# Performance work log

Hardware: AMD Instinct MI355X
Metric: run time of the kernel (lower is better)

The kernel has to match this reference:

```python
import jax, jax.numpy as jnp
import numpy as np
from jax import lax

GAMMA = 1.0  # init kwarg

def setup_inputs() -> dict:
    key = jax.random.key(0)
    k1, k2 = jax.random.split(key)
    B, L, D = 64, 256, 1024
    return {
        "student_tokens": jax.random.normal(k1, (B, L, D), jnp.float32),
        "teacher_tokens": jax.random.normal(k2, (B, L, D), jnp.float32),
    }

def _soft_dtw(dist, gamma):
    # dist: (B, LS, LT). Returns R[:, LS, LT] of the soft-DTW DP.
    B, LS, LT = dist.shape
    inf = jnp.array(jnp.inf, dist.dtype)

    def cell(r_left, inputs):
        d, r_diag, r_up = inputs  # each (B,)
        stacked = jnp.stack([r_diag, r_up, r_left], axis=-1)  # (B, 3)
        softmin = -gamma * jax.nn.logsumexp(-stacked / gamma, axis=-1)
        r = d + softmin
        return r, r

    def row_step(prev_row, dist_row):
        # prev_row: (B, LT+1) = R[i-1, :]; dist_row: (B, LT) = dist[:, i-1, :]
        xs = (dist_row.T, prev_row[:, :-1].T, prev_row[:, 1:].T)  # each (LT, B)
        r0 = jnp.full((B,), inf, dist.dtype)  # R[i, 0] = inf
        _, row = lax.scan(cell, r0, xs)  # (LT, B)
        new_row = jnp.concatenate([r0[:, None], row.T], axis=1)  # (B, LT+1)
        return new_row, None

    init_row = jnp.concatenate(
        [jnp.zeros((B, 1), dist.dtype), jnp.full((B, LT), inf, dist.dtype)], axis=1
    )  # R[0, :] = [0, inf, ..., inf]
    final_row, _ = lax.scan(row_step, init_row, jnp.swapaxes(dist, 0, 1))
    return final_row[:, -1]  # R[:, LS, LT]

def reference(student_tokens, teacher_tokens):
    # torch.cdist(p=2) via the expanded quadratic form (avoids (B,L,L,D) blowup)
    s2 = jnp.sum(student_tokens * student_tokens, axis=-1)  # (B, LS)
    t2 = jnp.sum(teacher_tokens * teacher_tokens, axis=-1)  # (B, LT)
    sq = (s2[:, :, None] + t2[:, None, :]
          - 2.0 * jnp.einsum('bld,bmd->blm', student_tokens, teacher_tokens))
    dist = jnp.sqrt(jnp.maximum(sq, 1e-12))  # (B, LS, LT)
    return _soft_dtw(dist, GAMMA).mean()
```

## Files before the change

### kernel.cpp

```cpp
#include <hip/hip_runtime.h>
#include <math.h>

#define BB 64
#define LL 256
#define DD 1024
#define NDPAD 512
#define BK 32
#define LOG2E 1.4426950408889634f
#define LN2   0.6931471805599453f

typedef __attribute__((ext_vector_type(8))) short short8v;
typedef __attribute__((ext_vector_type(4))) float float4v;

__device__ __forceinline__ unsigned short f2bf(float f) {
    unsigned u = __float_as_uint(f);
    unsigned r = (u + 0x7fffu + ((u >> 16) & 1u)) >> 16;
    return (unsigned short)r;
}
__device__ __forceinline__ float bf2f(unsigned short u) {
    return __uint_as_float(((unsigned)u) << 16);
}

__global__ __launch_bounds__(512) void fused_kernel(const float* __restrict__ S,
                                                    const float* __restrict__ T,
                                                    unsigned short* __restrict__ Dd) {
    __shared__ unsigned short lds[2][2][2][128 * BK];
    __shared__ float nrmP[2][2][128];

    const int b    = blockIdx.x;
    const int tile = blockIdx.y;
    const int i0 = (tile & 1) * 128;
    const int j0 = (tile >> 1) * 128;
    const int tid = threadIdx.x, w = tid >> 6, lane = tid & 63;
    const int p = w >> 2;
    const int q = w & 3;
    const int wr = q >> 1, wc = q & 1;
    const int kbase = p * 512;

    const float* Sg = S + ((size_t)b * LL + i0) * DD;
    const float* Tg = T + ((size_t)b * LL + j0) * DD;

    const int sr   = q * 16 + (lane >> 2);
    const int slot = lane & 3;
    const int kb   = slot ^ (sr & 3);

    float4v acc[4][4];
    const float4v fzero = {0.f, 0.f, 0.f, 0.f};
    #pragma unroll
    for (int mi = 0; mi < 4; ++mi)
        #pragma unroll
        for (int ni = 0; ni < 4; ++ni) acc[mi][ni] = fzero;

    struct Stg { float4 a[2][2]; float4 bb[2][2]; };
    Stg st0, st1;
    float ns[2][2] = {};

    auto issue = [&](Stg& s, int kt) {
        const float* pa = Sg + (size_t)sr * DD + kbase + kt * BK + kb * 8;
        const float* pb = Tg + (size_t)sr * DD + kbase + kt * BK + kb * 8;
        s.a[0][0]  = *(const float4*)(pa);
        s.a[0][1]  = *(const float4*)(pa + 4);
        s.a[1][0]  = *(const float4*)(pa + 64 * DD);
        s.a[1][1]  = *(const float4*)(pa + 64 * DD + 4);
        s.bb[0][0] = *(const float4*)(pb);
        s.bb[0][1] = *(const float4*)(pb + 4);
        s.bb[1][0] = *(const float4*)(pb + 64 * DD);
        s.bb[1][1] = *(const float4*)(pb + 64 * DD + 4);
    };

    auto cvtwrite = [&](const float4& v0, const float4& v1, unsigned short* dst, float& nacc) {
        nacc += v0.x * v0.x + v0.y * v0.y + v0.z * v0.z + v0.w * v0.w
              + v1.x * v1.x + v1.y * v1.y + v1.z * v1.z + v1.w * v1.w;
        uint4 o;
        o.x = ((unsigned)f2bf(v0.y) << 16) | f2bf(v0.x);
        o.y = ((unsigned)f2bf(v0.w) << 16) | f2bf(v0.z);
        o.z = ((unsigned)f2bf(v1.y) << 16) | f2bf(v1.x);
        o.w = ((unsigned)f2bf(v1.w) << 16) | f2bf(v1.z);
        *(uint4*)dst = o;
    };

    auto commit = [&](Stg& s, int buf) {
        #pragma unroll
        for (int n = 0; n < 2; ++n) {
            cvtwrite(s.a[n][0],  s.a[n][1],  &lds[p][buf][0][(n * 64 + sr) * BK + slot * 8], ns[0][n]);
            cvtwrite(s.bb[n][0], s.bb[n][1], &lds[p][buf][1][(n * 64 + sr) * BK + slot * 8], ns[1][n]);
        }
    };

    auto compute = [&](int buf) {
        const unsigned short* LA = &lds[p][buf][0][0];
        const unsigned short* LB = &lds[p][buf][1][0];
        short8v af[4], bf[4];
        #pragma unroll
        for (int mi = 0; mi < 4; ++mi) {
            int row = wr * 64 + mi * 16 + (lane & 15);
            int kbf = (lane >> 4) ^ (row & 3);
            af[mi] = *(const short8v*)(LA + row * BK + kbf * 8);
        }
        #pragma unroll
        for (int ni = 0; ni < 4; ++ni) {
            int row = wc * 64 + ni * 16 + (lane & 15);
            int kbf = (lane >> 4) ^ (row & 3);
            bf[ni] = *(const short8v*)(LB + row * BK + kbf * 8);
        }
        #pragma unroll
        for (int mi = 0; mi < 4; ++mi)
            #pragma unroll
            for (int ni = 0; ni < 4; ++ni)
                acc[mi][ni] = __builtin_amdgcn_mfma_f32_16x16x32_bf16(af[mi], bf[ni],
                                                                      acc[mi][ni], 0, 0, 0);
    };

    issue(st0, 0);
    for (int kt2 = 0; kt2 < 16; kt2 += 2) {
        issue(st1, kt2 + 1);
        commit(st0, 0);
        __syncthreads();
        compute(0);
        if (kt2 + 2 < 16) issue(st0, kt2 + 2);
        commit(st1, 1);
        __syncthreads();
        compute(1);
    }

    #pragma unroll
    for (int side = 0; side < 2; ++side)
        #pragma unroll
        for (int n = 0; n < 2; ++n) {
            float s = ns[side][n];
            s += __shfl_xor(s, 1, 64);
            s += __shfl_xor(s, 2, 64);
            if (slot == 0) nrmP[p][side][n * 64 + sr] = s;
        }
    __syncthreads();

    float* cb = (float*)&lds[0][0][0][0];
    if (p == 1) {
        #pragma unroll
        for (int mi = 0; mi < 4; ++mi)
            #pragma unroll
            for (int ni = 0; ni < 4; ++ni)
                *(float4v*)(cb + q * 4096 + (mi * 4 + ni) * 256 + lane * 4) = acc[mi][ni];
    }
    __syncthreads();

    if (p == 0) {
        #pragma unroll
        for (int mi = 0; mi < 4; ++mi)
            #pragma unroll
            for (int ni = 0; ni < 4; ++ni)
                acc[mi][ni] += *(const float4v*)(cb + q * 4096 + (mi * 4 + ni) * 256 + lane * 4);

        const int r0 = (lane >> 4) * 4;
        const int cf = lane & 15;
        unsigned short* Db = Dd + (size_t)b * NDPAD * 256;
        #pragma unroll
        for (int mi = 0; mi < 4; ++mi) {
            #pragma unroll
            for (int ni = 0; ni < 4; ++ni) {
                int lj = wc * 64 + ni * 16 + cf;
                float tj = nrmP[0][1][lj] + nrmP[1][1][lj];
                int j = j0 + lj;
                #pragma unroll
                for (int rg = 0; rg < 4; ++rg) {
                    int li = wr * 64 + mi * 16 + r0 + rg;
                    float sq = nrmP[0][0][li] + nrmP[1][0][li] + tj - 2.0f * acc[mi][ni][rg];
                    float dv = sqrtf(fmaxf(sq, 1e-12f));
                    int i = i0 + li;
                    Db[(size_t)(i + j) * 256 + j] = f2bf(dv * LOG2E);
                }
            }
        }
    }
}


__device__ __forceinline__ float wshr1(float src, float fill) {
    return __int_as_float(__builtin_amdgcn_update_dpp(
        __float_as_int(fill), __float_as_int(src), 0x138, 0xF, 0xF, false));
}

__global__ __launch_bounds__(256) void sdtw_kernel(const unsigned short* __restrict__ Dg,
                                                   float* __restrict__ res) {
    __shared__ unsigned short sd[8][16 * 256];
    __shared__ float bbuf[3][2][16];
    const int b = blockIdx.x;
    const int tid = threadIdx.x;
    const int w = tid >> 6;
    const int lane = tid & 63;
    const float INF = INFINITY;
    const unsigned short* Db = Dg + (size_t)b * NDPAD * 256;

    auto prefetch = [&](int c) {
        #pragma unroll
        for (int q = 0; q < 8; ++q) {
            __builtin_amdgcn_global_load_lds(
                (const __attribute__((address_space(1))) void*)(Db + (size_t)c * 4096 + q * 512 + lane * 8),
                (__attribute__((address_space(3))) void*)(&sd[c & 7][q * 512]),
                16, 0, 0);
        }
    };

    const int col0 = 64 * w + lane;
    float rm1 = INF, rm2 = INF;
    float p2carry = (tid == 0) ? 0.0f : INF;
    float bcarry = INF;

    if (w == 0) {
        prefetch(0);
        prefetch(1);
        asm volatile("s_waitcnt vmcnt(8)" ::: "memory");
    }
    asm volatile("s_waitcnt lgkmcnt(0)" ::: "memory");
    __builtin_amdgcn_s_barrier();

    for (int r = 0; r < 35; ++r) {
        if (w == 0 && r + 2 < 32) prefetch(r + 2);
        const int c = r - w;
        if (0 <= c && c < 32) {
            const unsigned short* Lp = &sd[c & 7][0];
            float dv[16];
            #pragma unroll
            for (int q = 0; q < 16; ++q)
                dv[q] = bf2f(Lp[q * 256 + col0]);

            float bv[16];
            if (w == 0) {
                #pragma unroll
                for (int q = 0; q < 16; ++q) bv[q] = INF;
            } else {
                const float4* bp4 = (const float4*)&bbuf[w - 1][c & 1][0];
                float4 b0 = bp4[0], b1 = bp4[1], b2 = bp4[2], b3 = bp4[3];
                bv[0] = bcarry;
                bv[1] = b0.x;  bv[2] = b0.y;  bv[3] = b0.z;  bv[4] = b0.w;
                bv[5] = b1.x;  bv[6] = b1.y;  bv[7] = b1.z;  bv[8] = b1.w;
                bv[9] = b2.x;  bv[10] = b2.y; bv[11] = b2.z; bv[12] = b2.w;
                bv[13] = b3.x; bv[14] = b3.y; bv[15] = b3.z;
                bcarry = b3.w;
            }
            asm volatile("s_waitcnt lgkmcnt(0)" ::: "memory");
            __builtin_amdgcn_sched_barrier(0);

            const int ibase = 16 * c - col0;
            float bb[16];
            #pragma unroll
            for (int q = 0; q < 16; ++q) {
                float p1 = wshr1(rm1, bv[q]);
                float p2 = p2carry;
                p2carry = p1;
                float m   = fminf(p2, fminf(rm1, p1));
                float mid = __builtin_amdgcn_fmed3f(p2, rm1, p1);
                float M   = fmaxf(p2, fmaxf(rm1, p1));
                float s   = (__builtin_amdgcn_exp2f(m - mid) +
                             __builtin_amdgcn_exp2f(m - M)) + 1.0f;
                float rcv = dv[q] + m - __builtin_amdgcn_logf(s);
                bool valid = (unsigned)(ibase + q) < 256u;
                rcv = valid ? rcv : INF;
                rm2 = rm1;
                rm1 = rcv;
                bb[q] = rcv;
            }
            if (w < 3 && lane == 63) {
                float4* op = (float4*)&bbuf[w][c & 1][0];
                op[0] = make_float4(bb[0], bb[1], bb[2], bb[3]);
                op[1] = make_float4(bb[4], bb[5], bb[6], bb[7]);
                op[2] = make_float4(bb[8], bb[9], bb[10], bb[11]);
                op[3] = make_float4(bb[12], bb[13], bb[14], bb[15]);
            }
        }
        if (w == 0) {
            if (r < 30) asm volatile("s_waitcnt vmcnt(8)" ::: "memory");
            else        asm volatile("s_waitcnt vmcnt(0)" ::: "memory");
        }
        asm volatile("s_waitcnt lgkmcnt(0)" ::: "memory");
        __builtin_amdgcn_s_barrier();
    }
    if (tid == 255) res[b] = rm2 * LN2;
}

__global__ void reduce_kernel(const float* __restrict__ res, float* __restrict__ out) {
    int t = threadIdx.x;
    float v = res[t];
    #pragma unroll
    for (int off = 32; off; off >>= 1) v += __shfl_down(v, off, 64);
    if (t == 0) out[0] = v * (1.0f / BB);
}

extern "C" void kernel_launch(void* const* d_in, const int* in_sizes, int n_in,
                              void* d_out, int out_size, void* d_ws, size_t ws_size,
                              hipStream_t stream) {
    const float* S = (const float*)d_in[0];
    const float* T = (const float*)d_in[1];

    const size_t nDiag = (size_t)BB * NDPAD * 256;
    unsigned short* diag = (unsigned short*)d_ws;
    float* rsv = (float*)(diag + nDiag);

    fused_kernel<<<dim3(BB, 4), 512, 0, stream>>>(S, T, diag);
    sdtw_kernel<<<BB, 256, 0, stream>>>(diag, rsv);
    reduce_kernel<<<1, 64, 0, stream>>>(rsv, (float*)d_out);
}
```

Before: 78.33 us.

## Stage fp32 tiles via direct global-to-LDS loads and convert to bf16 at fragment load

Replaces register-staged global loads plus bf16 conversion and LDS write with global_load_lds DMA of raw fp32 tiles into swizzled LDS. The bf16 conversion (now a packed v_cvt_pk_bf16_f32) and the row-norm accumulation move into the compute step, which reads fp32 fragments from LDS. The loop becomes a single-barrier double buffer. This is meant to cut VGPR staging and VALU work in the load path, but it doubles LDS footprint and read traffic, and it repeats the conversion for each wave that reads the same fragment.

```diff
diff --git a/kernel.cpp b/kernel.cpp
--- a/kernel.cpp
+++ b/kernel.cpp
@@ -5,12 +5,12 @@
 #define LL 256
 #define DD 1024
 #define NDPAD 512
-#define BK 32
 #define LOG2E 1.4426950408889634f
 #define LN2   0.6931471805599453f
 
 typedef __attribute__((ext_vector_type(8))) short short8v;
 typedef __attribute__((ext_vector_type(4))) float float4v;
+typedef __attribute__((ext_vector_type(4))) unsigned int uint4v;
 
 __device__ __forceinline__ unsigned short f2bf(float f) {
     unsigned u = __float_as_uint(f);
@@ -20,11 +20,16 @@
 __device__ __forceinline__ float bf2f(unsigned short u) {
     return __uint_as_float(((unsigned)u) << 16);
 }
+__device__ __forceinline__ unsigned cvtpk(float lo, float hi) {
+    unsigned r;
+    asm("v_cvt_pk_bf16_f32 %0, %1, %2" : "=v"(r) : "v"(lo), "v"(hi));
+    return r;
+}
 
 __global__ __launch_bounds__(512) void fused_kernel(const float* __restrict__ S,
                                                     const float* __restrict__ T,
                                                     unsigned short* __restrict__ Dd) {
-    __shared__ unsigned short lds[2][2][2][128 * BK];
+    __shared__ float lds[2][2][2][128 * 32];
     __shared__ float nrmP[2][2][128];
 
     const int b    = blockIdx.x;
@@ -40,9 +45,8 @@
     const float* Sg = S + ((size_t)b * LL + i0) * DD;
     const float* Tg = T + ((size_t)b * LL + j0) * DD;
 
-    const int sr   = q * 16 + (lane >> 2);
-    const int slot = lane & 3;
-    const int kb   = slot ^ (sr & 3);
+    const int srow = lane >> 3;
+    const int gsl  = lane & 7;
 
     float4v acc[4][4];
     const float4v fzero = {0.f, 0.f, 0.f, 0.f};
@@ -51,57 +55,56 @@
         #pragma unroll
         for (int ni = 0; ni < 4; ++ni) acc[mi][ni] = fzero;
 
-    struct Stg { float4 a[2][2]; float4 bb[2][2]; };
-    Stg st0, st1;
-    float ns[2][2] = {};
-
-    auto issue = [&](Stg& s, int kt) {
-        const float* pa = Sg + (size_t)sr * DD + kbase + kt * BK + kb * 8;
-        const float* pb = Tg + (size_t)sr * DD + kbase + kt * BK + kb * 8;
-        s.a[0][0]  = *(const float4*)(pa);
-        s.a[0][1]  = *(const float4*)(pa + 4);
-        s.a[1][0]  = *(const float4*)(pa + 64 * DD);
-        s.a[1][1]  = *(const float4*)(pa + 64 * DD + 4);
-        s.bb[0][0] = *(const float4*)(pb);
-        s.bb[0][1] = *(const float4*)(pb + 4);
-        s.bb[1][0] = *(const float4*)(pb + 64 * DD);
-        s.bb[1][1] = *(const float4*)(pb + 64 * DD + 4);
+    float nsA[4] = {0.f, 0.f, 0.f, 0.f};
+    float nsB[4] = {0.f, 0.f, 0.f, 0.f};
+
+    auto stage = [&](int buf, int kt) {
+        #pragma unroll
+        for (int o = 0; o < 4; ++o) {
+            int r  = q * 32 + o * 8 + srow;
+            int gs = gsl ^ (r & 7);
+            __builtin_amdgcn_global_load_lds(
+                (const __attribute__((address_space(1))) void*)(Sg + (size_t)r * DD + kbase + kt * 32 + gs * 4),
+                (__attribute__((address_space(3))) void*)(&lds[p][buf][0][(q * 32 + o * 8) * 32]),
+                16, 0, 0);
+            __builtin_amdgcn_global_load_lds(
+                (const __attribute__((address_space(1))) void*)(Tg + (size_t)r * DD + kbase + kt * 32 + gs * 4),
+                (__attribute__((address_space(3))) void*)(&lds[p][buf][1][(q * 32 + o * 8) * 32]),
+                16, 0, 0);
+        }
     };
 
-    auto cvtwrite = [&](const float4& v0, const float4& v1, unsigned short* dst, float& nacc) {
-        nacc += v0.x * v0.x + v0.y * v0.y + v0.z * v0.z + v0.w * v0.w
-              + v1.x * v1.x + v1.y * v1.y + v1.z * v1.z + v1.w * v1.w;
-        uint4 o;
-        o.x = ((unsigned)f2bf(v0.y) << 16) | f2bf(v0.x);
-        o.y = ((unsigned)f2bf(v0.w) << 16) | f2bf(v0.z);
-        o.z = ((unsigned)f2bf(v1.y) << 16) | f2bf(v1.x);
-        o.w = ((unsigned)f2bf(v1.w) << 16) | f2bf(v1.z);
-        *(uint4*)dst = o;
-    };
-
-    auto commit = [&](Stg& s, int buf) {
-        #pragma unroll
-        for (int n = 0; n < 2; ++n) {
-            cvtwrite(s.a[n][0],  s.a[n][1],  &lds[p][buf][0][(n * 64 + sr) * BK + slot * 8], ns[0][n]);
-            cvtwrite(s.bb[n][0], s.bb[n][1], &lds[p][buf][1][(n * 64 + sr) * BK + slot * 8], ns[1][n]);
-        }
-    };
+    const int j2 = (lane >> 4) * 2;
 
     auto compute = [&](int buf) {
-        const unsigned short* LA = &lds[p][buf][0][0];
-        const unsigned short* LB = &lds[p][buf][1][0];
+        const float* LA = &lds[p][buf][0][0];
+        const float* LB = &lds[p][buf][1][0];
         short8v af[4], bf[4];
         #pragma unroll
         for (int mi = 0; mi < 4; ++mi) {
-            int row = wr * 64 + mi * 16 + (lane & 15);
-            int kbf = (lane >> 4) ^ (row & 3);
-            af[mi] = *(const short8v*)(LA + row * BK + kbf * 8);
+            int r = wr * 64 + mi * 16 + (lane & 15);
+            float4 e0 = *(const float4*)(LA + r * 32 + ((j2    ) ^ (r & 7)) * 4);
+            float4 e1 = *(const float4*)(LA + r * 32 + ((j2 + 1) ^ (r & 7)) * 4);
+            if (wc == 0)
+                nsA[mi] += e0.x * e0.x + e0.y * e0.y + e0.z * e0.z + e0.w * e0.w
+                         + e1.x * e1.x + e1.y * e1.y + e1.z * e1.z + e1.w * e1.w;
+            union { uint4v u; short8v s; } cv;
+            cv.u[0] = cvtpk(e0.x, e0.y); cv.u[1] = cvtpk(e0.z, e0.w);
+            cv.u[2] = cvtpk(e1.x, e1.y); cv.u[3] = cvtpk(e1.z, e1.w);
+            af[mi] = cv.s;
         }
         #pragma unroll
         for (int ni = 0; ni < 4; ++ni) {
-            int row = wc * 64 + ni * 16 + (lane & 15);
-            int kbf = (lane >> 4) ^ (row & 3);
-            bf[ni] = *(const short8v*)(LB + row * BK + kbf * 8);
+            int r = wc * 64 + ni * 16 + (lane & 15);
+            float4 e0 = *(const float4*)(LB + r * 32 + ((j2    ) ^ (r & 7)) * 4);
+            float4 e1 = *(const float4*)(LB + r * 32 + ((j2 + 1) ^ (r & 7)) * 4);
+            if (wr == 0)
+                nsB[ni] += e0.x * e0.x + e0.y * e0.y + e0.z * e0.z + e0.w * e0.w
+                         + e1.x * e1.x + e1.y * e1.y + e1.z * e1.z + e1.w * e1.w;
+            union { uint4v u; short8v s; } cv;
+            cv.u[0] = cvtpk(e0.x, e0.y); cv.u[1] = cvtpk(e0.z, e0.w);
+            cv.u[2] = cvtpk(e1.x, e1.y); cv.u[3] = cvtpk(e1.z, e1.w);
+            bf[ni] = cv.s;
         }
         #pragma unroll
         for (int mi = 0; mi < 4; ++mi)
@@ -111,30 +114,35 @@
                                                                       acc[mi][ni], 0, 0, 0);
     };
 
-    issue(st0, 0);
-    for (int kt2 = 0; kt2 < 16; kt2 += 2) {
-        issue(st1, kt2 + 1);
-        commit(st0, 0);
+    stage(0, 0);
+    for (int kt = 0; kt < 16; ++kt) {
+        int cur = kt & 1;
         __syncthreads();
-        compute(0);
-        if (kt2 + 2 < 16) issue(st0, kt2 + 2);
-        commit(st1, 1);
-        __syncthreads();
-        compute(1);
-    }
-
-    #pragma unroll
-    for (int side = 0; side < 2; ++side)
-        #pragma unroll
-        for (int n = 0; n < 2; ++n) {
-            float s = ns[side][n];
-            s += __shfl_xor(s, 1, 64);
-            s += __shfl_xor(s, 2, 64);
-            if (slot == 0) nrmP[p][side][n * 64 + sr] = s;
-        }
+        if (kt < 15) stage(cur ^ 1, kt + 1);
+        compute(cur);
+    }
+
+    if (wc == 0) {
+        #pragma unroll
+        for (int mi = 0; mi < 4; ++mi) {
+            float s = nsA[mi];
+            s += __shfl_xor(s, 16, 64);
+            s += __shfl_xor(s, 32, 64);
+            if (lane < 16) nrmP[p][0][wr * 64 + mi * 16 + lane] = s;
+        }
+    }
+    if (wr == 0) {
+        #pragma unroll
+        for (int ni = 0; ni < 4; ++ni) {
+            float s = nsB[ni];
+            s += __shfl_xor(s, 16, 64);
+            s += __shfl_xor(s, 32, 64);
+            if (lane < 16) nrmP[p][1][wc * 64 + ni * 16 + lane] = s;
+        }
+    }
     __syncthreads();
 
-    float* cb = (float*)&lds[0][0][0][0];
+    float* cb = &lds[0][0][0][0];
     if (p == 1) {
         #pragma unroll
         for (int mi = 0; mi < 4; ++mi)
```

Result: slower. 85.00 us (+8.5%).
